# Kernel optimization log

Hardware: AMD Instinct MI355X
Metric: run time of the kernel (lower is better)

The kernel has to match this reference:

```python
import jax, jax.numpy as jnp
import numpy as np

H_HEADS = 32
KV_HEADS = 8
HEAD_DIM = 64  # hidden // num_heads = 2048 // 32


def setup_inputs() -> dict:
    key = jax.random.key(0)
    ks = jax.random.split(key, 5)
    B, T, hidden = 2, 2048, 2048
    kv_dim = KV_HEADS * HEAD_DIM
    s = 0.02
    return {
        "x": jax.random.normal(ks[0], (B, T, hidden), dtype=jnp.float32),
        "Wq": jax.random.normal(ks[1], (hidden, hidden), dtype=jnp.float32) * s,
        "Wk": jax.random.normal(ks[2], (hidden, kv_dim), dtype=jnp.float32) * s,
        "Wv": jax.random.normal(ks[3], (hidden, kv_dim), dtype=jnp.float32) * s,
        "Wo": jax.random.normal(ks[4], (hidden, hidden), dtype=jnp.float32) * s,
    }


def reference(x, Wq, Wk, Wv, Wo):
    B, T, hidden = x.shape
    h, kv, d = H_HEADS, KV_HEADS, HEAD_DIM
    g = h // kv  # GQA group size
    scale = d ** (-0.5)

    # projections
    q = (x @ Wq).reshape(B, T, h, d).transpose(0, 2, 1, 3)        # [B,h,T,d]
    k = (x @ Wk).reshape(B, T, kv, d).transpose(0, 2, 1, 3)      # [B,kv,T,d]
    v = (x @ Wv).reshape(B, T, kv, d).transpose(0, 2, 1, 3)      # [B,kv,T,d]

    # native GQA broadcast: group q heads by their shared kv head
    # (equivalent math to torch repeat_interleave on k/v)
    qg = q.reshape(B, kv, g, T, d)                                # [B,kv,g,T,d]
    scores = jnp.einsum("bkgtd,bksd->bkgts", qg, k) * scale       # [B,kv,g,T,T]
    attn = jax.nn.softmax(scores, axis=-1)
    og = jnp.einsum("bkgts,bksd->bkgtd", attn, v)                 # [B,kv,g,T,d]
    out = og.reshape(B, h, T, d).transpose(0, 2, 1, 3).reshape(B, T, h * d)
    return out @ Wo
```

## Files before the change

kernel.cpp:

```cpp
#include <hip/hip_runtime.h>

#define AS1 __attribute__((address_space(1)))
#define AS3 __attribute__((address_space(3)))

typedef unsigned short u16;
typedef unsigned int u32;
typedef __attribute__((ext_vector_type(8))) _Float16 half8;
typedef __attribute__((ext_vector_type(2))) _Float16 half2v;
typedef __attribute__((ext_vector_type(4))) u16 u16x4;
typedef __attribute__((ext_vector_type(4))) u32 u32x4;
typedef __attribute__((ext_vector_type(4))) float f32x4;
typedef __attribute__((ext_vector_type(16))) float f32x16;

__device__ __forceinline__ u16 f2h(float f) {
    _Float16 h = (_Float16)f;
    return __builtin_bit_cast(u16, h);
}

__device__ __forceinline__ u32 pk2h(float a, float b) {
    return __builtin_bit_cast(u32, __builtin_amdgcn_cvt_pkrtz(a, b));
}

__device__ __forceinline__ float fexp2(float x) {
#if __has_builtin(__builtin_amdgcn_exp2f)
    return __builtin_amdgcn_exp2f(x);
#else
    return __expf(x * 0.69314718055994531f);
#endif
}

__device__ __forceinline__ float dot2acc(u32 w, float acc) {
#if __has_builtin(__builtin_amdgcn_fdot2)
    half2v ones = { (_Float16)1.f, (_Float16)1.f };
    return __builtin_amdgcn_fdot2(__builtin_bit_cast(half2v, w), ones, acc, false);
#else
    half2v p = __builtin_bit_cast(half2v, w);
    return acc + (float)p[0] + (float)p[1];
#endif
}

__device__ __forceinline__ void plswap(u32& a, u32& b) {
    asm("v_permlane32_swap_b32 %0, %1" : "+v"(a), "+v"(b));
}

__device__ __forceinline__ void async16(const void* g, void* l) {
    __builtin_amdgcn_global_load_lds((AS1 void*)g, (AS3 void*)l, 16, 0, 0);
}


__global__ void cast_f32_to_f16(const float* __restrict__ in, u16* __restrict__ out) {
    int i = (blockIdx.x * 256 + threadIdx.x) * 4;
    float4 v = *(const float4*)(in + i);
    u16x4 o = { f2h(v.x), f2h(v.y), f2h(v.z), f2h(v.w) };
    *(u16x4*)(out + i) = o;
}

__global__ void transpose_cast(const float* __restrict__ in, u16* __restrict__ out,
                               int K, int N, float scale) {
    __shared__ float tile[32][33];
    int nb = blockIdx.x * 32, kb = blockIdx.y * 32;
    int tx = threadIdx.x & 31, ty = threadIdx.x >> 5;
#pragma unroll
    for (int r = ty; r < 32; r += 8)
        tile[r][tx] = in[(size_t)(kb + r) * N + nb + tx];
    __syncthreads();
#pragma unroll
    for (int r = ty; r < 32; r += 8)
        out[(size_t)(nb + r) * K + kb + tx] = f2h(tile[tx][r] * scale);
}


template <int OUTMODE>
__global__ __launch_bounds__(256, 2) void gemm_bt(const u16* __restrict__ A,
                                                  const u16* __restrict__ Bt,
                                                  void* __restrict__ C,
                                                  void* __restrict__ C2,
                                                  int M, int N, int K, int ldc) {
    __shared__ __align__(16) u16 As[2][128 * 32];
    __shared__ __align__(16) u16 Bs[2][128 * 32];
    const int m0 = blockIdx.x * 128, n0 = blockIdx.y * 128;
    const int wave = threadIdx.x >> 6, lane = threadIdx.x & 63;
    const int quad = lane >> 4, mm = lane & 15;
    const int wm = (wave >> 1) * 64, wn = (wave & 1) * 64;

    const int srow = wave * 16 + (lane >> 2);
    const int scol = 8 * ((lane & 3) ^ ((lane >> 3) & 3));

    const u16* ag0 = A + (size_t)(m0 + srow) * K + scol;
    const u16* ag1 = A + (size_t)(m0 + 64 + srow) * K + scol;
    const u16* bg0 = Bt + (size_t)(n0 + srow) * K + scol;
    const u16* bg1 = Bt + (size_t)(n0 + 64 + srow) * K + scol;
    const int soff = wave * 512 + lane * 8;

    f32x4 acc[4][4] = {};
    const int swz = (mm >> 1) & 3;

#define GST(buf)                                                              \
    {                                                                         \
        u16* ad = &As[buf][soff];                                             \
        u16* bd = &Bs[buf][soff];                                             \
        async16(ag0, ad);                                                     \
        async16(ag1, ad + 2048);                                              \
        async16(bg0, bd);                                                     \
        async16(bg1, bd + 2048);                                              \
        ag0 += 32; ag1 += 32; bg0 += 32; bg1 += 32;                           \
    }

    GST(0);
    int cur = 0;

    for (int k0 = 0; k0 < K; k0 += 32) {
        __syncthreads();
        if (k0 + 32 < K) GST(cur ^ 1);
        const u16* Ac = &As[cur][0];
        const u16* Bc = &Bs[cur][0];
        half8 af[4], bf[4];
#pragma unroll
        for (int i = 0; i < 4; i++)
            af[i] = *(const half8*)(Ac + (wm + i * 16 + mm) * 32 + (quad ^ swz) * 8);
#pragma unroll
        for (int i = 0; i < 4; i++)
            bf[i] = *(const half8*)(Bc + (wn + i * 16 + mm) * 32 + (quad ^ swz) * 8);
#pragma unroll
        for (int mi = 0; mi < 4; mi++)
#pragma unroll
            for (int ni = 0; ni < 4; ni++)
                acc[mi][ni] = __builtin_amdgcn_mfma_f32_16x16x32_f16(
                    af[mi], bf[ni], acc[mi][ni], 0, 0, 0);
        cur ^= 1;
    }
#undef GST

    if (OUTMODE == 0) {
        float* Cp = (float*)C;
#pragma unroll
        for (int mi = 0; mi < 4; mi++)
#pragma unroll
            for (int r = 0; r < 4; r++) {
                float* rp = Cp + (size_t)(m0 + wm + mi * 16 + quad * 4 + r) * ldc + n0 + wn + mm;
#pragma unroll
                for (int ni = 0; ni < 4; ni++) rp[ni * 16] = acc[mi][ni][r];
            }
    } else if (OUTMODE == 1) {
        u16* Cp = (u16*)C;
#pragma unroll
        for (int mi = 0; mi < 4; mi++)
#pragma unroll
            for (int r = 0; r < 4; r++) {
                u16* rp = Cp + (size_t)(m0 + wm + mi * 16 + quad * 4 + r) * ldc + n0 + wn + mm;
#pragma unroll
                for (int ni = 0; ni < 4; ni++) rp[ni * 16] = f2h(acc[mi][ni][r]);
            }
    } else if (OUTMODE == 2) {
        u16* Cp = (u16*)C;
#pragma unroll
        for (int mi = 0; mi < 4; mi++)
#pragma unroll
            for (int r = 0; r < 4; r++) {
                int row = m0 + wm + mi * 16 + quad * 4 + r;
#pragma unroll
                for (int ni = 0; ni < 4; ni++)
                    Cp[(size_t)(n0 + wn + ni * 16 + mm) * ldc + row] = f2h(acc[mi][ni][r]);
            }
    } else {
        if (n0 < 512) {
            u16* Cp = (u16*)C;
#pragma unroll
            for (int mi = 0; mi < 4; mi++)
#pragma unroll
                for (int r = 0; r < 4; r++) {
                    u16* rp = Cp + (size_t)(m0 + wm + mi * 16 + quad * 4 + r) * 512 + n0 + wn + mm;
#pragma unroll
                    for (int ni = 0; ni < 4; ni++) rp[ni * 16] = f2h(acc[mi][ni][r]);
                }
        } else {
            u16* Cp = (u16*)C2;
#pragma unroll
            for (int mi = 0; mi < 4; mi++)
#pragma unroll
                for (int r = 0; r < 4; r++) {
                    int row = m0 + wm + mi * 16 + quad * 4 + r;
#pragma unroll
                    for (int ni = 0; ni < 4; ni++)
                        Cp[(size_t)(n0 - 512 + wn + ni * 16 + mm) * 4096 + row] = f2h(acc[mi][ni][r]);
                }
        }
    }
}


template <int SPLIT>
__global__ __launch_bounds__(256, 4) void attn_fwd(const u16* __restrict__ Qb,
                                                   const u16* __restrict__ Kb,
                                                   const u16* __restrict__ Vtb,
                                                   u16* __restrict__ Ob,
                                                   float* __restrict__ Of0,
                                                   float* __restrict__ Of1,
                                                   float* __restrict__ Lf) {
    __shared__ __align__(16) u16 Ks[2][64 * 64];
    __shared__ __align__(16) u16 Vs[2][64 * 64];

    const int qtb = blockIdx.x, head = blockIdx.y;
    const int b = blockIdx.z & 1, sp = blockIdx.z >> 1;
    const int kvh = head >> 2;
    const int wave = threadIdx.x >> 6, lane = threadIdx.x & 63;
    const int h = lane >> 5;
    const int q32 = lane & 31;
    const int t = threadIdx.x;

    const size_t qrow0 = (size_t)b * 2048 + qtb * 128 + wave * 32;
    const int s_beg = sp * (2048 / SPLIT), s_end = s_beg + 2048 / SPLIT;

    half8 qf[4];
#pragma unroll
    for (int s = 0; s < 4; s++)
        qf[s] = *(const half8*)(Qb + (qrow0 + q32) * 2048 + head * 64 + s * 16 + h * 8);

    f32x16 accO[2] = {};
    float lp0 = 0.f, lp1 = 0.f;

    const int srow = t >> 3;
    const int lch = (t & 7) ^ (srow & 7);
    const u16* kg = Kb + ((size_t)b * 2048 + srow) * 512 + kvh * 64 + lch * 8;
    const u16* vg = Vtb + ((size_t)kvh * 64 + srow) * 4096 + b * 2048 + lch * 8;

#define STAGE(buf, s0)                                                        \
    {                                                                         \
        u16* kd = &Ks[buf][t * 8];                                            \
        u16* vd = &Vs[buf][t * 8];                                            \
        async16(kg + (size_t)(s0) * 512, kd);                                 \
        async16(kg + (size_t)((s0) + 32) * 512, kd + 2048);                   \
        async16(vg + (s0), vd);                                               \
        async16(vg + (size_t)32 * 4096 + (s0), vd + 2048);                    \
    }

    int cur = 0;
    STAGE(0, s_beg);

    const int r0 = q32, r1 = 32 + q32;
    const int sw0 = (r0 & 7), sw1 = (r1 & 7);

    for (int s0 = s_beg; s0 < s_end; s0 += 64) {
        __syncthreads();
        int sn = s0 + 64;
        if (sn < s_end) STAGE(cur ^ 1, sn);

        const u16* Kc = &Ks[cur][0];
        const u16* Vc = &Vs[cur][0];
        const u16* Kr0 = Kc + r0 * 64;
        const u16* Kr1 = Kc + r1 * 64;

        f32x16 a0, a1;
#pragma unroll
        for (int i = 0; i < 16; i++) { a0[i] = -10.f; a1[i] = -10.f; }

        __builtin_amdgcn_s_setprio(1);
#pragma unroll
        for (int s = 0; s < 4; s++) {
            half8 k0 = *(const half8*)(Kr0 + (((2 * s + h) ^ sw0) << 3));
            a0 = __builtin_amdgcn_mfma_f32_32x32x16_f16(k0, qf[s], a0, 0, 0, 0);
            half8 k1 = *(const half8*)(Kr1 + (((2 * s + h) ^ sw1) << 3));
            a1 = __builtin_amdgcn_mfma_f32_32x32x16_f16(k1, qf[s], a1, 0, 0, 0);
        }
        __builtin_amdgcn_s_setprio(0);

        u32 w0[8];
#pragma unroll
        for (int m = 0; m < 8; m++) {
            w0[m] = pk2h(fexp2(a0[2 * m]), fexp2(a0[2 * m + 1]));
            lp0 = dot2acc(w0[m], lp0);
        }

        __builtin_amdgcn_s_setprio(1);
#pragma unroll
        for (int k1 = 0; k1 < 2; k1++) {
            const int ks = k1;
            u32 d0 = w0[4 * k1 + 0], d2 = w0[4 * k1 + 2];
            u32 d1 = w0[4 * k1 + 1], d3 = w0[4 * k1 + 3];
            plswap(d0, d2);
            plswap(d1, d3);
            u32x4 pd = { d0, d1, d2, d3 };
            half8 pf = __builtin_bit_cast(half8, pd);
#pragma unroll
            for (int dt = 0; dt < 2; dt++) {
                const int rv = dt * 32 + q32;
                half8 vf = *(const half8*)(&Vc[rv * 64 + (((2 * ks + h) ^ (rv & 7)) << 3)]);
                accO[dt] = __builtin_amdgcn_mfma_f32_32x32x16_f16(vf, pf, accO[dt], 0, 0, 0);
            }
        }
        __builtin_amdgcn_s_setprio(0);

        u32 w1[8];
#pragma unroll
        for (int m = 0; m < 8; m++) {
            w1[m] = pk2h(fexp2(a1[2 * m]), fexp2(a1[2 * m + 1]));
            lp1 = dot2acc(w1[m], lp1);
        }

        __builtin_amdgcn_s_setprio(1);
#pragma unroll
        for (int k1 = 0; k1 < 2; k1++) {
            const int ks = 2 + k1;
            u32 d0 = w1[4 * k1 + 0], d2 = w1[4 * k1 + 2];
            u32 d1 = w1[4 * k1 + 1], d3 = w1[4 * k1 + 3];
            plswap(d0, d2);
            plswap(d1, d3);
            u32x4 pd = { d0, d1, d2, d3 };
            half8 pf = __builtin_bit_cast(half8, pd);
#pragma unroll
            for (int dt = 0; dt < 2; dt++) {
                const int rv = dt * 32 + q32;
                half8 vf = *(const half8*)(&Vc[rv * 64 + (((2 * ks + h) ^ (rv & 7)) << 3)]);
                accO[dt] = __builtin_amdgcn_mfma_f32_32x32x16_f16(vf, pf, accO[dt], 0, 0, 0);
            }
        }
        __builtin_amdgcn_s_setprio(0);

        cur ^= 1;
    }
#undef STAGE

    float l = lp0 + lp1;
    l += __shfl_xor(l, 32);

    const size_t token = qrow0 + q32;
    if (SPLIT == 1) {
        float inv = 1.f / l;
#pragma unroll
        for (int dt = 0; dt < 2; dt++)
#pragma unroll
            for (int rq = 0; rq < 4; rq++) {
                u16x4 o = { f2h(accO[dt][4 * rq + 0] * inv), f2h(accO[dt][4 * rq + 1] * inv),
                            f2h(accO[dt][4 * rq + 2] * inv), f2h(accO[dt][4 * rq + 3] * inv) };
                *(u16x4*)(Ob + token * 2048 + head * 64 + dt * 32 + rq * 8 + h * 4) = o;
            }
    } else {
        float* Op = sp ? Of1 : Of0;
#pragma unroll
        for (int dt = 0; dt < 2; dt++)
#pragma unroll
            for (int rq = 0; rq < 4; rq++) {
                f32x4 o = { accO[dt][4 * rq + 0], accO[dt][4 * rq + 1],
                            accO[dt][4 * rq + 2], accO[dt][4 * rq + 3] };
                *(f32x4*)(Op + token * 2048 + head * 64 + dt * 32 + rq * 8 + h * 4) = o;
            }
        if (!h) Lf[((size_t)sp * 4096 + token) * 32 + head] = l;
    }
}


extern "C" void kernel_launch(void* const* d_in, const int* in_sizes, int n_in,
                              void* d_out, int out_size, void* d_ws, size_t ws_size,
                              hipStream_t stream) {
    (void)in_sizes; (void)n_in; (void)out_size; (void)ws_size;
    const float* x  = (const float*)d_in[0];
    const float* Wq = (const float*)d_in[1];
    const float* Wk = (const float*)d_in[2];
    const float* Wv = (const float*)d_in[3];
    const float* Wo = (const float*)d_in[4];
    float* out = (float*)d_out;

    u16* ws = (u16*)d_ws;
    u16* xb   = ws;
    u16* Wqt  = xb   + (size_t)4096 * 2048;
    u16* Wkvt = Wqt  + (size_t)2048 * 2048;
    u16* Wot  = Wkvt + (size_t)1024 * 2048;
    u16* Qb   = Wot  + (size_t)2048 * 2048;
    u16* Kb   = Qb   + (size_t)4096 * 2048;
    u16* Vtb  = Kb   + (size_t)4096 * 512;
    u16* Ob   = Vtb  + (size_t)512 * 4096;

    const float qscale = 0.125f * 1.4426950408889634f;

    cast_f32_to_f16<<<8192, 256, 0, stream>>>(x, xb);
    transpose_cast<<<dim3(64, 64), 256, 0, stream>>>(Wq, Wqt, 2048, 2048, qscale);
    transpose_cast<<<dim3(16, 64), 256, 0, stream>>>(Wk, Wkvt, 2048, 512, 1.f);
    transpose_cast<<<dim3(16, 64), 256, 0, stream>>>(Wv, Wkvt + (size_t)512 * 2048, 2048, 512, 1.f);
    transpose_cast<<<dim3(64, 64), 256, 0, stream>>>(Wo, Wot, 2048, 2048, 1.f);

    gemm_bt<1><<<dim3(32, 16), 256, 0, stream>>>(xb, Wqt, Qb, nullptr, 4096, 2048, 2048, 2048);
    gemm_bt<3><<<dim3(32, 8),  256, 0, stream>>>(xb, Wkvt, Kb, Vtb, 4096, 1024, 2048, 512);

    attn_fwd<1><<<dim3(16, 32, 2), 256, 0, stream>>>(Qb, Kb, Vtb, Ob,
                                                     nullptr, nullptr, nullptr);

    gemm_bt<0><<<dim3(32, 16), 256, 0, stream>>>(Ob, Wot, out, nullptr, 4096, 2048, 2048, 2048);
}
```

Baseline: 341.0 us.

## Fuse Q and KV projections into one GEMM, split softmax row-sum accumulators

Merges the separate Q projection and KV projection GEMM launches into a single gemm_bt<3> launch over N=3072, relying on Wqt and Wkvt being contiguous in the workspace and on Kb/Vtb sitting right after each other. The epilogue now routes column tiles to Q, K, or transposed V outputs. This removes one launch and the tail imbalance of two smaller grids, and the launch bound is raised to 3 blocks per SM for this mode. In attention, the setprio hints are dropped and the row-sum accumulation is spread over four independent accumulators to shorten the dependency chain.

```diff
diff --git a/kernel.cpp b/kernel.cpp
--- a/kernel.cpp
+++ b/kernel.cpp
@@ -71,11 +71,10 @@
 
 
 template <int OUTMODE>
-__global__ __launch_bounds__(256, 2) void gemm_bt(const u16* __restrict__ A,
-                                                  const u16* __restrict__ Bt,
-                                                  void* __restrict__ C,
-                                                  void* __restrict__ C2,
-                                                  int M, int N, int K, int ldc) {
+__global__ __launch_bounds__(256, OUTMODE == 3 ? 3 : 2) void gemm_bt(
+        const u16* __restrict__ A, const u16* __restrict__ Bt,
+        void* __restrict__ C, void* __restrict__ C2,
+        int M, int N, int K, int ldc) {
     __shared__ __align__(16) u16 As[2][128 * 32];
     __shared__ __align__(16) u16 Bs[2][128 * 32];
     const int m0 = blockIdx.x * 128, n0 = blockIdx.y * 128;
@@ -163,18 +162,28 @@
                     Cp[(size_t)(n0 + wn + ni * 16 + mm) * ldc + row] = f2h(acc[mi][ni][r]);
             }
     } else {
-        if (n0 < 512) {
-            u16* Cp = (u16*)C;
+        if (n0 < 2048) {
+            u16* Qp = (u16*)C;
 #pragma unroll
             for (int mi = 0; mi < 4; mi++)
 #pragma unroll
                 for (int r = 0; r < 4; r++) {
-                    u16* rp = Cp + (size_t)(m0 + wm + mi * 16 + quad * 4 + r) * 512 + n0 + wn + mm;
+                    u16* rp = Qp + (size_t)(m0 + wm + mi * 16 + quad * 4 + r) * 2048 + n0 + wn + mm;
+#pragma unroll
+                    for (int ni = 0; ni < 4; ni++) rp[ni * 16] = f2h(acc[mi][ni][r]);
+                }
+        } else if (n0 < 2560) {
+            u16* Kp = (u16*)C2;
+#pragma unroll
+            for (int mi = 0; mi < 4; mi++)
+#pragma unroll
+                for (int r = 0; r < 4; r++) {
+                    u16* rp = Kp + (size_t)(m0 + wm + mi * 16 + quad * 4 + r) * 512 + (n0 - 2048) + wn + mm;
 #pragma unroll
                     for (int ni = 0; ni < 4; ni++) rp[ni * 16] = f2h(acc[mi][ni][r]);
                 }
         } else {
-            u16* Cp = (u16*)C2;
+            u16* Vp = (u16*)C2 + (size_t)4096 * 512;
 #pragma unroll
             for (int mi = 0; mi < 4; mi++)
 #pragma unroll
@@ -182,7 +191,7 @@
                     int row = m0 + wm + mi * 16 + quad * 4 + r;
 #pragma unroll
                     for (int ni = 0; ni < 4; ni++)
-                        Cp[(size_t)(n0 - 512 + wn + ni * 16 + mm) * 4096 + row] = f2h(acc[mi][ni][r]);
+                        Vp[(size_t)(n0 - 2560 + wn + ni * 16 + mm) * 4096 + row] = f2h(acc[mi][ni][r]);
                 }
         }
     }
@@ -217,7 +226,7 @@
         qf[s] = *(const half8*)(Qb + (qrow0 + q32) * 2048 + head * 64 + s * 16 + h * 8);
 
     f32x16 accO[2] = {};
-    float lp0 = 0.f, lp1 = 0.f;
+    float lpq[4] = {0.f, 0.f, 0.f, 0.f};
 
     const int srow = t >> 3;
     const int lch = (t & 7) ^ (srow & 7);
@@ -254,7 +263,6 @@
 #pragma unroll
         for (int i = 0; i < 16; i++) { a0[i] = -10.f; a1[i] = -10.f; }
 
-        __builtin_amdgcn_s_setprio(1);
 #pragma unroll
         for (int s = 0; s < 4; s++) {
             half8 k0 = *(const half8*)(Kr0 + (((2 * s + h) ^ sw0) << 3));
@@ -262,16 +270,14 @@
             half8 k1 = *(const half8*)(Kr1 + (((2 * s + h) ^ sw1) << 3));
             a1 = __builtin_amdgcn_mfma_f32_32x32x16_f16(k1, qf[s], a1, 0, 0, 0);
         }
-        __builtin_amdgcn_s_setprio(0);
 
         u32 w0[8];
 #pragma unroll
         for (int m = 0; m < 8; m++) {
             w0[m] = pk2h(fexp2(a0[2 * m]), fexp2(a0[2 * m + 1]));
-            lp0 = dot2acc(w0[m], lp0);
-        }
-
-        __builtin_amdgcn_s_setprio(1);
+            lpq[m & 3] = dot2acc(w0[m], lpq[m & 3]);
+        }
+
 #pragma unroll
         for (int k1 = 0; k1 < 2; k1++) {
             const int ks = k1;
@@ -288,16 +294,14 @@
                 accO[dt] = __builtin_amdgcn_mfma_f32_32x32x16_f16(vf, pf, accO[dt], 0, 0, 0);
             }
         }
-        __builtin_amdgcn_s_setprio(0);
 
         u32 w1[8];
 #pragma unroll
         for (int m = 0; m < 8; m++) {
             w1[m] = pk2h(fexp2(a1[2 * m]), fexp2(a1[2 * m + 1]));
-            lp1 = dot2acc(w1[m], lp1);
-        }
-
-        __builtin_amdgcn_s_setprio(1);
+            lpq[m & 3] = dot2acc(w1[m], lpq[m & 3]);
+        }
+
 #pragma unroll
         for (int k1 = 0; k1 < 2; k1++) {
             const int ks = 2 + k1;
@@ -314,13 +318,12 @@
                 accO[dt] = __builtin_amdgcn_mfma_f32_32x32x16_f16(vf, pf, accO[dt], 0, 0, 0);
             }
         }
-        __builtin_amdgcn_s_setprio(0);
 
         cur ^= 1;
     }
 #undef STAGE
 
-    float l = lp0 + lp1;
+    float l = (lpq[0] + lpq[1]) + (lpq[2] + lpq[3]);
     l += __shfl_xor(l, 32);
 
     const size_t token = qrow0 + q32;
@@ -378,8 +381,7 @@
     transpose_cast<<<dim3(16, 64), 256, 0, stream>>>(Wv, Wkvt + (size_t)512 * 2048, 2048, 512, 1.f);
     transpose_cast<<<dim3(64, 64), 256, 0, stream>>>(Wo, Wot, 2048, 2048, 1.f);
 
-    gemm_bt<1><<<dim3(32, 16), 256, 0, stream>>>(xb, Wqt, Qb, nullptr, 4096, 2048, 2048, 2048);
-    gemm_bt<3><<<dim3(32, 8),  256, 0, stream>>>(xb, Wkvt, Kb, Vtb, 4096, 1024, 2048, 512);
+    gemm_bt<3><<<dim3(32, 24), 256, 0, stream>>>(xb, Wqt, Qb, Kb, 4096, 3072, 2048, 2048);
 
     attn_fwd<1><<<dim3(16, 32, 2), 256, 0, stream>>>(Qb, Kb, Vtb, Ob,
                                                      nullptr, nullptr, nullptr);
```

New measurement: 312.1 us. -8.5%, faster.
